# Optimization experiments

Measured on AMD Instinct MI355X. Metric: run time of the kernel, lower is better.

The kernel has to match this reference:

```python
import jax, jax.numpy as jnp
import numpy as np

NV, NQ, K, C, FF, H = 40000, 8192, 96, 128, 256, 8
DH = C // H


def _layernorm(x, g, b, eps=1e-5):
    m = jnp.mean(x, axis=-1, keepdims=True)
    v = jnp.var(x, axis=-1, keepdims=True)
    return (x - m) * jax.lax.rsqrt(v + eps) * g + b


def setup_inputs() -> dict:
    key = jax.random.key(0)
    ks = jax.random.split(key, 20)
    voxel_features = jax.random.normal(ks[0], (NV, C), dtype=jnp.float32)
    voxel_coords = jax.random.normal(ks[1], (NV, 3), dtype=jnp.float32)
    query_coords = jax.random.normal(ks[2], (NQ, 3), dtype=jnp.float32)
    raw = jax.random.randint(ks[3], (NQ, K), 0, 50000)
    key_indices = jnp.where(raw >= NV, -1, raw)  # -1 marks padded/missing keys
    key_indices = key_indices.at[:, 0].set(raw[:, 0] % NV)  # ensure >=1 valid key per query
    w = lambda k, shape: (jax.random.normal(k, shape, dtype=jnp.float32) * 0.02)
    return {
        "voxel_features": voxel_features,
        "voxel_coords": voxel_coords,
        "query_coords": query_coords,
        "key_indices": key_indices,
        "norm1_g": jnp.ones((C,), jnp.float32), "norm1_b": jnp.zeros((C,), jnp.float32),
        "q_pos_w": w(ks[4], (C, 3)), "q_pos_b": jnp.zeros((C,), jnp.float32),
        "k_pos_w": w(ks[5], (C, 3)), "k_pos_b": jnp.zeros((C,), jnp.float32),
        "in_w": w(ks[6], (3 * C, C)), "in_b": jnp.zeros((3 * C,), jnp.float32),
        "out_w": w(ks[7], (C, C)), "out_b": jnp.zeros((C,), jnp.float32),
        "norm2_g": jnp.ones((C,), jnp.float32), "norm2_b": jnp.zeros((C,), jnp.float32),
        "lin1_w": w(ks[8], (FF, C)), "lin1_b": jnp.zeros((FF,), jnp.float32),
        "lin2_w": w(ks[9], (C, FF)), "lin2_b": jnp.zeros((C,), jnp.float32),
        "fin_w": w(ks[10], (C, C)), "fin_b": jnp.zeros((C,), jnp.float32),
    }


def reference(voxel_features, voxel_coords, query_coords, key_indices,
              norm1_g, norm1_b, q_pos_w, q_pos_b, k_pos_w, k_pos_b,
              in_w, in_b, out_w, out_b, norm2_g, norm2_b,
              lin1_w, lin1_b, lin2_w, lin2_b, fin_w, fin_b):
    mask = key_indices < 0                      # [NQ, K] True = padded
    idx = jnp.where(mask, 0, key_indices)
    vf = _layernorm(voxel_features, norm1_g, norm1_b)   # norm1
    key_feat = vf[idx]                          # gather: [NQ, K, C]
    key_c = voxel_coords[idx]                   # [NQ, K, 3]
    # q_pos_proj: Linear(3,C)+ReLU ; k_pos_proj: Conv1d(3,C,1)+ReLU (== per-key linear)
    q_feat = jax.nn.relu(query_coords @ q_pos_w.T + q_pos_b)        # [NQ, C]
    key_pos = jax.nn.relu(jnp.einsum('nkt,ct->nkc', key_c, k_pos_w) + k_pos_b)
    key_feat = key_feat + key_pos               # [NQ, K, C]
    # nn.MultiheadAttention: query [1,NQ,C], key/value [K,NQ,C] -> per-query attention over K keys
    wq, wk, wv = in_w[:C], in_w[C:2 * C], in_w[2 * C:]
    bq, bk, bv = in_b[:C], in_b[C:2 * C], in_b[2 * C:]
    q = (q_feat @ wq.T + bq).reshape(NQ, H, DH)                 # [NQ,H,DH]
    k = (key_feat @ wk.T + bk).reshape(NQ, K, H, DH)            # [NQ,K,H,DH]
    v = (key_feat @ wv.T + bv).reshape(NQ, K, H, DH)
    scale = 1.0 / np.sqrt(DH)
    scores = jnp.einsum('nhd,nkhd->nhk', q, k) * scale          # [NQ,H,K]
    scores = jnp.where(mask[:, None, :], jnp.float32(-1e9), scores)
    attn = jax.nn.softmax(scores, axis=-1)
    ctx = jnp.einsum('nhk,nkhd->nhd', attn, v).reshape(NQ, C)
    attend = ctx @ out_w.T + out_b                              # [NQ,C]
    # FFN block (dropout=0 -> identity)
    h = _layernorm(attend, norm2_g, norm2_b)
    act = jax.nn.relu(h @ lin1_w.T + lin1_b) @ lin2_w.T + lin2_b
    x = attend + act
    out = jax.nn.relu(x @ fin_w.T + fin_b)                      # output_layer
    return out
```

## Files before the change

### kernel.cpp

```cpp
#include <hip/hip_runtime.h>
#include <hip/hip_bf16.h>
#include <math.h>

constexpr int NVOX = 40000;
constexpr int NQRY = 8192;
constexpr int KK   = 96;
constexpr int CH   = 128;
constexpr int FFD  = 256;

typedef __attribute__((ext_vector_type(8))) short short8;
typedef __attribute__((ext_vector_type(4))) float float4v;

__device__ inline float bflo(unsigned u) { return __uint_as_float(u << 16); }
__device__ inline float bfhi(unsigned u) { return __uint_as_float(u & 0xffff0000u); }
__device__ inline unsigned short f2bf(float x) {
  union { float f; unsigned u; } a; a.f = x;
  const unsigned r = a.u + 0x7fffu + ((a.u >> 16) & 1u);
  return (unsigned short)(r >> 16);
}
__device__ inline unsigned pack2(float lo, float hi) {
  return (unsigned)f2bf(lo) | ((unsigned)f2bf(hi) << 16);
}

__global__ __launch_bounds__(256) void k_prep(
    const float* __restrict__ vfeat, const float* __restrict__ vcoord,
    const float* __restrict__ n1g, const float* __restrict__ n1b,
    const float* __restrict__ kpw, const float* __restrict__ kpb,
    const float* __restrict__ in_w,
    const float* __restrict__ ow, const float* __restrict__ l1w,
    const float* __restrict__ l2w, const float* __restrict__ fw,
    __hip_bfloat16* __restrict__ Gb, __hip_bfloat16* __restrict__ Wb,
    __hip_bfloat16* __restrict__ Eb) {
  const int b = blockIdx.x;
  const int t = threadIdx.x;
  if (b < NVOX/16) {
    const int vloc = t >> 4;
    const int l    = t & 15;
    const int j = b * 16 + vloc;
    const float4* vrow = reinterpret_cast<const float4*>(vfeat + (size_t)j * CH);
    const float4 x0 = vrow[l*2], x1 = vrow[l*2+1];
    float s  = x0.x+x0.y+x0.z+x0.w + x1.x+x1.y+x1.z+x1.w;
    float ss = x0.x*x0.x+x0.y*x0.y+x0.z*x0.z+x0.w*x0.w
             + x1.x*x1.x+x1.y*x1.y+x1.z*x1.z+x1.w*x1.w;
    #pragma unroll
    for (int m = 8; m >= 1; m >>= 1) { s += __shfl_xor(s, m); ss += __shfl_xor(ss, m); }
    const float mean = s * (1.0f/CH);
    const float var  = ss * (1.0f/CH) - mean*mean;
    const float rstd = 1.0f / sqrtf(var + 1e-5f);
    const float c0 = vcoord[j*3+0], c1 = vcoord[j*3+1], c2 = vcoord[j*3+2];
    const float xv[8] = {x0.x,x0.y,x0.z,x0.w,x1.x,x1.y,x1.z,x1.w};
    float gv[8];
    #pragma unroll
    for (int u = 0; u < 8; u++) {
      const int c = l*8 + u;
      const float vf = (xv[u] - mean) * rstd * n1g[c] + n1b[c];
      const float kp = fmaf(c0, kpw[c*3+0], fmaf(c1, kpw[c*3+1], fmaf(c2, kpw[c*3+2], kpb[c])));
      gv[u] = vf + fmaxf(kp, 0.0f);
    }
    const uint4 pk = make_uint4(pack2(gv[0],gv[1]), pack2(gv[2],gv[3]),
                                pack2(gv[4],gv[5]), pack2(gv[6],gv[7]));
    *reinterpret_cast<uint4*>(Gb + (size_t)j*CH + l*8) = pk;
  } else {
    const int idx = b - NVOX/16;
    const float* src;
    __hip_bfloat16* dst;
    if (idx < 8) {
      const int e = (idx * 256 + t) * 16;
      src = in_w + (size_t)CH*CH + e;
      dst = Wb + e;
    } else {
      const int f = ((idx - 8) * 256 + t) * 16;
      dst = Eb + f;
      if      (f < 16384) src = ow  + f;
      else if (f < 49152) src = l1w + (f - 16384);
      else if (f < 81920) src = l2w + (f - 49152);
      else                src = fw  + (f - 81920);
    }
    float v[16];
    #pragma unroll
    for (int u = 0; u < 4; u++) {
      const float4 fq = *reinterpret_cast<const float4*>(src + u*4);
      v[u*4+0]=fq.x; v[u*4+1]=fq.y; v[u*4+2]=fq.z; v[u*4+3]=fq.w;
    }
    uint4* o = reinterpret_cast<uint4*>(dst);
    o[0] = make_uint4(pack2(v[0],v[1]), pack2(v[2],v[3]),
                      pack2(v[4],v[5]), pack2(v[6],v[7]));
    o[1] = make_uint4(pack2(v[8],v[9]), pack2(v[10],v[11]),
                      pack2(v[12],v[13]), pack2(v[14],v[15]));
  }
}

__global__ __launch_bounds__(256) void k_kv_gemm(
    const __hip_bfloat16* __restrict__ Gb, const __hip_bfloat16* __restrict__ Wb,
    const float* __restrict__ in_b,
    unsigned short* __restrict__ KVh) {
  __shared__ unsigned short ldsD[64][72];
  const int t = threadIdx.x;
  const int w = t >> 6;
  const int lane = t & 63;
  const int col = lane & 15;
  const int quad = lane >> 4;
  const int bx = blockIdx.x;
  const int v0 = (bx >> 2) * 64;
  const int cg = bx & 3;

  const unsigned short* gRow =
      reinterpret_cast<const unsigned short*>(Gb) + (size_t)(v0 + w*16 + col)*CH + quad*8;
  short8 afrag[4];
  #pragma unroll
  for (int kq = 0; kq < 4; kq++)
    afrag[kq] = *reinterpret_cast<const short8*>(gRow + kq*32);

  float4v acc[4];
  #pragma unroll
  for (int j = 0; j < 4; j++) {
    const float bia = in_b[CH + cg*64 + j*16 + col];
    acc[j] = (float4v){bia, bia, bia, bia};
  }
  const unsigned short* wB = reinterpret_cast<const unsigned short*>(Wb);
  #pragma unroll
  for (int kq = 0; kq < 4; kq++) {
    #pragma unroll
    for (int j = 0; j < 4; j++) {
      const short8 bfrag = *reinterpret_cast<const short8*>(
          wB + (size_t)(cg*64 + j*16 + col)*CH + kq*32 + quad*8);
      acc[j] = __builtin_amdgcn_mfma_f32_16x16x32_bf16(afrag[kq], bfrag, acc[j], 0, 0, 0);
    }
  }
  #pragma unroll
  for (int j = 0; j < 4; j++)
    #pragma unroll
    for (int r = 0; r < 4; r++)
      ldsD[w*16 + quad*4 + r][j*16 + col] = f2bf(acc[j][r]);
  __syncthreads();
  const int row = t >> 2;
  const int cc  = (t & 3) * 16;
  const uint4 d0 = *reinterpret_cast<const uint4*>(&ldsD[row][cc]);
  const uint4 d1 = *reinterpret_cast<const uint4*>(&ldsD[row][cc+8]);
  const int head = (cg & 1) * 4 + (cc >> 4);
  const int isV  = cg >> 1;
  unsigned short* dst = KVh + ((size_t)head*NVOX + (v0 + row))*32 + isV*16;
  uint4* out = reinterpret_cast<uint4*>(dst);
  out[0] = d0; out[1] = d1;
}

__global__ __launch_bounds__(256) void k_query(
    const float* __restrict__ qcoord,
    const float* __restrict__ qpw, const float* __restrict__ qpb,
    const float* __restrict__ in_w, const float* __restrict__ in_b,
    float* __restrict__ qout) {
  __shared__ float qf[16][CH];
  const int t = threadIdx.x;
  const int qbase = blockIdx.x * 16;
  #pragma unroll
  for (int i = 0; i < 8; i++) {
    const int e = t + 256*i;
    const int qv = e >> 7, c = e & 127;
    const int qq = qbase + qv;
    const float v = fmaf(qcoord[qq*3+0], qpw[c*3+0],
                    fmaf(qcoord[qq*3+1], qpw[c*3+1],
                    fmaf(qcoord[qq*3+2], qpw[c*3+2], qpb[c])));
    qf[qv][c] = fmaxf(v, 0.0f);
  }
  __syncthreads();
  const int oc = t & 127, half = t >> 7;
  const float* wrow = in_w + (size_t)oc * CH;
  const float bia = in_b[oc];
  float acc[8];
  #pragma unroll
  for (int v = 0; v < 8; v++) acc[v] = bia;
  for (int c = 0; c < CH; c += 4) {
    const float4 w4 = *reinterpret_cast<const float4*>(wrow + c);
    #pragma unroll
    for (int v = 0; v < 8; v++) {
      const float4 g4 = *reinterpret_cast<const float4*>(&qf[half*8+v][c]);
      acc[v] = fmaf(g4.x, w4.x, fmaf(g4.y, w4.y, fmaf(g4.z, w4.z, fmaf(g4.w, w4.w, acc[v]))));
    }
  }
  #pragma unroll
  for (int v = 0; v < 8; v++) qout[(size_t)(qbase + half*8 + v)*CH + oc] = acc[v];
}

__global__ __launch_bounds__(256) void k_attn(
    const unsigned short* __restrict__ KVh,
    const float* __restrict__ qg, const int* __restrict__ kidx,
    float* __restrict__ ctxg) {
  __shared__ float qs[8][16];
  __shared__ int   js[8*KK];
  __shared__ float sc[8*KK];
  __shared__ float red[4][8][16];
  __shared__ float rden[8];
  const int t  = threadIdx.x;
  const int h  = blockIdx.x & 7;
  const int n0 = (blockIdx.x >> 3) * 8;
  const unsigned short* KVbase = KVh + (size_t)h * NVOX * 32;

  #pragma unroll
  for (int i = 0; i < 3; i++)
    js[t + 256*i] = kidx[(size_t)n0*KK + t + 256*i];
  if (t < 128) {
    const int q = t >> 4, d = t & 15;
    qs[q][d] = qg[(size_t)(n0 + q)*CH + h*16 + d];
  }
  __syncthreads();
  #pragma unroll
  for (int i = 0; i < 3; i++) {
    const int e = t + 256*i;
    const int q = e / KK, k = e - q*KK;
    const int j = js[e];
    float s;
    if (j < 0) {
      s = -1e9f;
    } else {
      const uint4* kr = reinterpret_cast<const uint4*>(KVbase + (size_t)j*32);
      const uint4 ka = kr[0], kb = kr[1];
      const float* qh = qs[q];
      s = 0.0f;
      s = fmaf(qh[0],  bflo(ka.x), s); s = fmaf(qh[1],  bfhi(ka.x), s);
      s = fmaf(qh[2],  bflo(ka.y), s); s = fmaf(qh[3],  bfhi(ka.y), s);
      s = fmaf(qh[4],  bflo(ka.z), s); s = fmaf(qh[5],  bfhi(ka.z), s);
      s = fmaf(qh[6],  bflo(ka.w), s); s = fmaf(qh[7],  bfhi(ka.w), s);
      s = fmaf(qh[8],  bflo(kb.x), s); s = fmaf(qh[9],  bfhi(kb.x), s);
      s = fmaf(qh[10], bflo(kb.y), s); s = fmaf(qh[11], bfhi(kb.y), s);
      s = fmaf(qh[12], bflo(kb.z), s); s = fmaf(qh[13], bfhi(kb.z), s);
      s = fmaf(qh[14], bflo(kb.w), s); s = fmaf(qh[15], bfhi(kb.w), s);
      s *= 0.25f;
    }
    sc[e] = s;
  }
  __syncthreads();
  if (t < 128) {
    const int q = t >> 4, l = t & 15;
    float mx = -3e38f;
    for (int k = l; k < KK; k += 16) mx = fmaxf(mx, sc[q*KK + k]);
    #pragma unroll
    for (int m = 8; m >= 1; m >>= 1) mx = fmaxf(mx, __shfl_xor(mx, m));
    float sum = 0.0f;
    for (int k = l; k < KK; k += 16) {
      const float p = __expf(sc[q*KK + k] - mx);
      sc[q*KK + k] = p;
      sum += p;
    }
    #pragma unroll
    for (int m = 8; m >= 1; m >>= 1) sum += __shfl_xor(sum, m);
    if (l == 0) rden[q] = 1.0f / sum;
  }
  __syncthreads();
  {
    const int q = t >> 5, cp = (t >> 2) & 7, kg = t & 3;
    float a0 = 0.0f, a1 = 0.0f;
    const int k0 = kg * 24;
    for (int k = k0; k < k0 + 24; k++) {
      const int j = js[q*KK + k];
      if (j >= 0) {
        const unsigned vv = *reinterpret_cast<const unsigned*>(
            KVbase + (size_t)j*32 + 16 + cp*2);
        const float w = sc[q*KK + k];
        a0 = fmaf(w, bflo(vv), a0);
        a1 = fmaf(w, bfhi(vv), a1);
      }
    }
    *reinterpret_cast<float2*>(&red[kg][q][cp*2]) = make_float2(a0, a1);
  }
  __syncthreads();
  if (t < 128) {
    const int q = t >> 4, d = t & 15;
    ctxg[(size_t)(n0 + q)*CH + h*16 + d] =
        (red[0][q][d] + red[1][q][d] + red[2][q][d] + red[3][q][d]) * rden[q];
  }
}

__global__ __launch_bounds__(256) void k_epi(
    const float* __restrict__ ctxg, const __hip_bfloat16* __restrict__ Eb,
    const float* __restrict__ ob,
    const float* __restrict__ n2g, const float* __restrict__ n2b,
    const float* __restrict__ l1b, const float* __restrict__ l2b,
    const float* __restrict__ fb,
    float* __restrict__ outp) {
  __shared__ unsigned short csb[16][136];
  __shared__ float attnS[16][132];
  __shared__ unsigned short hb[16][136];
  __shared__ unsigned short a1b[16][264];
  __shared__ unsigned short xb[16][136];
  const unsigned short* owb  = reinterpret_cast<const unsigned short*>(Eb);
  const unsigned short* l1wb = owb + 16384;
  const unsigned short* l2wb = owb + 49152;
  const unsigned short* fwb  = owb + 81920;

  const int t = threadIdx.x;
  const int w = t >> 6;
  const int lane = t & 63;
  const int col = lane & 15;
  const int quad = lane >> 4;
  const int qbase = blockIdx.x * 16;

  {
    const int e = t * 8;
    const int row = e >> 7, cc = e & 127;
    const float4* src = reinterpret_cast<const float4*>(ctxg + (size_t)(qbase+row)*CH + cc);
    const float4 x0 = src[0], x1 = src[1];
    *reinterpret_cast<uint4*>(&csb[row][cc]) =
        make_uint4(pack2(x0.x,x0.y), pack2(x0.z,x0.w), pack2(x1.x,x1.y), pack2(x1.z,x1.w));
  }
  __syncthreads();
  {
    short8 af[4];
    #pragma unroll
    for (int kq = 0; kq < 4; kq++)
      af[kq] = *reinterpret_cast<const short8*>(&csb[col][quad*8 + kq*32]);
    #pragma unroll
    for (int j = 0; j < 2; j++) {
      const int n0 = w*32 + j*16;
      const float bia = ob[n0 + col];
      float4v acc = (float4v){bia, bia, bia, bia};
      #pragma unroll
      for (int kq = 0; kq < 4; kq++) {
        const short8 bf = *reinterpret_cast<const short8*>(
            owb + (size_t)(n0 + col)*CH + kq*32 + quad*8);
        acc = __builtin_amdgcn_mfma_f32_16x16x32_bf16(af[kq], bf, acc, 0, 0, 0);
      }
      #pragma unroll
      for (int r = 0; r < 4; r++) attnS[quad*4 + r][n0 + col] = acc[r];
    }
  }
  __syncthreads();
  {
    const int row = t >> 4, l = t & 15;
    float s = 0.0f, ss = 0.0f;
    #pragma unroll
    for (int c = l; c < CH; c += 16) { const float x = attnS[row][c]; s += x; ss += x*x; }
    #pragma unroll
    for (int m = 8; m >= 1; m >>= 1) { s += __shfl_xor(s, m); ss += __shfl_xor(ss, m); }
    const float mean = s * (1.0f/CH);
    const float var  = ss * (1.0f/CH) - mean*mean;
    const float rstd = 1.0f / sqrtf(var + 1e-5f);
    #pragma unroll
    for (int c = l; c < CH; c += 16)
      hb[row][c] = f2bf((attnS[row][c] - mean) * rstd * n2g[c] + n2b[c]);
  }
  __syncthreads();
  {
    short8 af[4];
    #pragma unroll
    for (int kq = 0; kq < 4; kq++)
      af[kq] = *reinterpret_cast<const short8*>(&hb[col][quad*8 + kq*32]);
    #pragma unroll
    for (int j = 0; j < 4; j++) {
      const int n0 = w*64 + j*16;
      const float bia = l1b[n0 + col];
      float4v acc = (float4v){bia, bia, bia, bia};
      #pragma unroll
      for (int kq = 0; kq < 4; kq++) {
        const short8 bf = *reinterpret_cast<const short8*>(
            l1wb + (size_t)(n0 + col)*CH + kq*32 + quad*8);
        acc = __builtin_amdgcn_mfma_f32_16x16x32_bf16(af[kq], bf, acc, 0, 0, 0);
      }
      #pragma unroll
      for (int r = 0; r < 4; r++)
        a1b[quad*4 + r][n0 + col] = f2bf(fmaxf(acc[r], 0.0f));
    }
  }
  __syncthreads();
  {
    short8 af[8];
    #pragma unroll
    for (int kq = 0; kq < 8; kq++)
      af[kq] = *reinterpret_cast<const short8*>(&a1b[col][quad*8 + kq*32]);
    #pragma unroll
    for (int j = 0; j < 2; j++) {
      const int n0 = w*32 + j*16;
      const float bia = l2b[n0 + col];
      float4v acc = (float4v){bia, bia, bia, bia};
      #pragma unroll
      for (int kq = 0; kq < 8; kq++) {
        const short8 bf = *reinterpret_cast<const short8*>(
            l2wb + (size_t)(n0 + col)*FFD + kq*32 + quad*8);
        acc = __builtin_amdgcn_mfma_f32_16x16x32_bf16(af[kq], bf, acc, 0, 0, 0);
      }
      #pragma unroll
      for (int r = 0; r < 4; r++)
        xb[quad*4 + r][n0 + col] = f2bf(acc[r] + attnS[quad*4 + r][n0 + col]);
    }
  }
  __syncthreads();
  {
    short8 af[4];
    #pragma unroll
    for (int kq = 0; kq < 4; kq++)
      af[kq] = *reinterpret_cast<const short8*>(&xb[col][quad*8 + kq*32]);
    #pragma unroll
    for (int j = 0; j < 2; j++) {
      const int n0 = w*32 + j*16;
      const float bia = fb[n0 + col];
      float4v acc = (float4v){bia, bia, bia, bia};
      #pragma unroll
      for (int kq = 0; kq < 4; kq++) {
        const short8 bf = *reinterpret_cast<const short8*>(
            fwb + (size_t)(n0 + col)*CH + kq*32 + quad*8);
        acc = __builtin_amdgcn_mfma_f32_16x16x32_bf16(af[kq], bf, acc, 0, 0, 0);
      }
      #pragma unroll
      for (int r = 0; r < 4; r++)
        outp[(size_t)(qbase + quad*4 + r)*CH + n0 + col] = fmaxf(acc[r], 0.0f);
    }
  }
}

extern "C" void kernel_launch(void* const* d_in, const int* in_sizes, int n_in,
                              void* d_out, int out_size, void* d_ws, size_t ws_size,
                              hipStream_t stream) {
  const float* vfeat  = (const float*)d_in[0];
  const float* vcoord = (const float*)d_in[1];
  const float* qcoord = (const float*)d_in[2];
  const int*   kidx   = (const int*)  d_in[3];
  const float* n1g    = (const float*)d_in[4];
  const float* n1b    = (const float*)d_in[5];
  const float* qpw    = (const float*)d_in[6];
  const float* qpb    = (const float*)d_in[7];
  const float* kpw    = (const float*)d_in[8];
  const float* kpb    = (const float*)d_in[9];
  const float* in_w   = (const float*)d_in[10];
  const float* in_b   = (const float*)d_in[11];
  const float* out_w  = (const float*)d_in[12];
  const float* out_b  = (const float*)d_in[13];
  const float* n2g    = (const float*)d_in[14];
  const float* n2b    = (const float*)d_in[15];
  const float* l1w    = (const float*)d_in[16];
  const float* l1b    = (const float*)d_in[17];
  const float* l2w    = (const float*)d_in[18];
  const float* l2b    = (const float*)d_in[19];
  const float* fw     = (const float*)d_in[20];
  const float* fb     = (const float*)d_in[21];
  float* out = (float*)d_out;

  unsigned short* KVh = (unsigned short*)d_ws;
  __hip_bfloat16* Gb = (__hip_bfloat16*)(KVh + (size_t)8*NVOX*32);
  __hip_bfloat16* Wb = Gb + (size_t)NVOX*CH;
  __hip_bfloat16* Eb = Wb + (size_t)2*CH*CH;
  float* qb = (float*)(Eb + 98304);
  float* cx = qb + (size_t)NQRY*CH;

  k_prep   <<<NVOX/16 + 32, 256, 0, stream>>>(vfeat, vcoord, n1g, n1b, kpw, kpb,
                                              in_w, out_w, l1w, l2w, fw, Gb, Wb, Eb);
  k_query  <<<NQRY/16, 256, 0, stream>>>(qcoord, qpw, qpb, in_w, in_b, qb);
  k_kv_gemm<<<(NVOX/64)*4, 256, 0, stream>>>(Gb, Wb, in_b, KVh);
  k_attn   <<<(NQRY/8)*8, 256, 0, stream>>>(KVh, qb, kidx, cx);
  k_epi    <<<NQRY/16, 256, 0, stream>>>(cx, Eb, out_b, n2g, n2b, l1b, l2b, fb, out);
}
```

Measured before the change: 226.6 us.

## Load each key/value row once into registers and reuse it for scores and context

The attention kernel now has each group of 4 lanes load a full 64-byte K/V row with coalesced 16-byte loads. All 12 rows per thread are issued up front and kept in registers. Scores are computed from those registers with a lane shuffle, and the same registers are reused for the weighted V sum. This removes the second gather of V from global memory and the staging of key indices in shared memory. The cost is higher register pressure (48 extra VGPRs for the buffer) and more redundant FMAs on masked keys, which are clamped to row 0.

Result: faster. 209.6 us (-7.5%).

```diff
diff --git a/kernel.cpp b/kernel.cpp
--- a/kernel.cpp
+++ b/kernel.cpp
@@ -186,59 +186,63 @@
     const float* __restrict__ qg, const int* __restrict__ kidx,
     float* __restrict__ ctxg) {
   __shared__ float qs[8][16];
-  __shared__ int   js[8*KK];
-  __shared__ float sc[8*KK];
-  __shared__ float red[4][8][16];
+  __shared__ float sc[8*104];
+  __shared__ float red[128][9];
   __shared__ float rden[8];
-  const int t  = threadIdx.x;
-  const int h  = blockIdx.x & 7;
-  const int n0 = (blockIdx.x >> 3) * 8;
+  const int t    = threadIdx.x;
+  const int h    = blockIdx.x & 7;
+  const int n0   = (blockIdx.x >> 3) * 8;
+  const int w    = t >> 6;
+  const int lane = t & 63;
+  const int quad = lane >> 2;
+  const int r    = lane & 3;
+  const int qh   = quad >> 3;
+  const int g    = quad & 7;
+  const int q_l  = 2*w + qh;
   const unsigned short* KVbase = KVh + (size_t)h * NVOX * 32;
 
-  #pragma unroll
-  for (int i = 0; i < 3; i++)
-    js[t + 256*i] = kidx[(size_t)n0*KK + t + 256*i];
   if (t < 128) {
     const int q = t >> 4, d = t & 15;
     qs[q][d] = qg[(size_t)(n0 + q)*CH + h*16 + d];
   }
-  __syncthreads();
-  #pragma unroll
-  for (int i = 0; i < 3; i++) {
-    const int e = t + 256*i;
-    const int q = e / KK, k = e - q*KK;
-    const int j = js[e];
-    float s;
-    if (j < 0) {
-      s = -1e9f;
-    } else {
-      const uint4* kr = reinterpret_cast<const uint4*>(KVbase + (size_t)j*32);
-      const uint4 ka = kr[0], kb = kr[1];
-      const float* qh = qs[q];
-      s = 0.0f;
-      s = fmaf(qh[0],  bflo(ka.x), s); s = fmaf(qh[1],  bfhi(ka.x), s);
-      s = fmaf(qh[2],  bflo(ka.y), s); s = fmaf(qh[3],  bfhi(ka.y), s);
-      s = fmaf(qh[4],  bflo(ka.z), s); s = fmaf(qh[5],  bfhi(ka.z), s);
-      s = fmaf(qh[6],  bflo(ka.w), s); s = fmaf(qh[7],  bfhi(ka.w), s);
-      s = fmaf(qh[8],  bflo(kb.x), s); s = fmaf(qh[9],  bfhi(kb.x), s);
-      s = fmaf(qh[10], bflo(kb.y), s); s = fmaf(qh[11], bfhi(kb.y), s);
-      s = fmaf(qh[12], bflo(kb.z), s); s = fmaf(qh[13], bfhi(kb.z), s);
-      s = fmaf(qh[14], bflo(kb.w), s); s = fmaf(qh[15], bfhi(kb.w), s);
-      s *= 0.25f;
-    }
-    sc[e] = s;
+  unsigned msk = 0;
+  uint4 kvbuf[12];
+  const int krow = (n0 + q_l)*KK + g;
+  #pragma unroll
+  for (int it = 0; it < 12; it++) {
+    const int j0 = kidx[krow + it*8];
+    msk |= (unsigned)(j0 < 0) << it;
+    const int j = (j0 < 0) ? 0 : j0;
+    kvbuf[it] = *reinterpret_cast<const uint4*>(KVbase + (size_t)j*32 + r*8);
+  }
+  __syncthreads();
+  const float4 qa = *reinterpret_cast<const float4*>(&qs[q_l][(r & 1)*8]);
+  const float4 qb = *reinterpret_cast<const float4*>(&qs[q_l][(r & 1)*8 + 4]);
+  #pragma unroll
+  for (int it = 0; it < 12; it++) {
+    const uint4 kv = kvbuf[it];
+    float s = 0.0f;
+    s = fmaf(qa.x, bflo(kv.x), s); s = fmaf(qa.y, bfhi(kv.x), s);
+    s = fmaf(qa.z, bflo(kv.y), s); s = fmaf(qa.w, bfhi(kv.y), s);
+    s = fmaf(qb.x, bflo(kv.z), s); s = fmaf(qb.y, bfhi(kv.z), s);
+    s = fmaf(qb.z, bflo(kv.w), s); s = fmaf(qb.w, bfhi(kv.w), s);
+    s += __shfl_xor(s, 1);
+    if (r == 0)
+      sc[q_l*104 + g + it*8] = ((msk >> it) & 1) ? -1e9f : s * 0.25f;
   }
   __syncthreads();
   if (t < 128) {
     const int q = t >> 4, l = t & 15;
     float mx = -3e38f;
-    for (int k = l; k < KK; k += 16) mx = fmaxf(mx, sc[q*KK + k]);
+    #pragma unroll
+    for (int k = l; k < KK; k += 16) mx = fmaxf(mx, sc[q*104 + k]);
     #pragma unroll
     for (int m = 8; m >= 1; m >>= 1) mx = fmaxf(mx, __shfl_xor(mx, m));
     float sum = 0.0f;
+    #pragma unroll
     for (int k = l; k < KK; k += 16) {
-      const float p = __expf(sc[q*KK + k] - mx);
-      sc[q*KK + k] = p;
+      const float p = __expf(sc[q*104 + k] - mx);
+      sc[q*104 + k] = p;
       sum += p;
     }
     #pragma unroll
@@ -247,26 +251,30 @@
   }
   __syncthreads();
   {
-    const int q = t >> 5, cp = (t >> 2) & 7, kg = t & 3;
-    float a0 = 0.0f, a1 = 0.0f;
-    const int k0 = kg * 24;
-    for (int k = k0; k < k0 + 24; k++) {
-      const int j = js[q*KK + k];
-      if (j >= 0) {
-        const unsigned vv = *reinterpret_cast<const unsigned*>(
-            KVbase + (size_t)j*32 + 16 + cp*2);
-        const float w = sc[q*KK + k];
-        a0 = fmaf(w, bflo(vv), a0);
-        a1 = fmaf(w, bfhi(vv), a1);
-      }
-    }
-    *reinterpret_cast<float2*>(&red[kg][q][cp*2]) = make_float2(a0, a1);
+    float acc[8] = {0,0,0,0,0,0,0,0};
+    #pragma unroll
+    for (int it = 0; it < 12; it++) {
+      const float wg = sc[q_l*104 + g + it*8];
+      const uint4 kv = kvbuf[it];
+      acc[0] = fmaf(wg, bflo(kv.x), acc[0]); acc[1] = fmaf(wg, bfhi(kv.x), acc[1]);
+      acc[2] = fmaf(wg, bflo(kv.y), acc[2]); acc[3] = fmaf(wg, bfhi(kv.y), acc[3]);
+      acc[4] = fmaf(wg, bflo(kv.z), acc[4]); acc[5] = fmaf(wg, bfhi(kv.z), acc[5]);
+      acc[6] = fmaf(wg, bflo(kv.w), acc[6]); acc[7] = fmaf(wg, bfhi(kv.w), acc[7]);
+    }
+    if (r >= 2) {
+      const int slot = q_l*16 + g*2 + (r - 2);
+      #pragma unroll
+      for (int u = 0; u < 8; u++) red[slot][u] = acc[u];
+    }
   }
   __syncthreads();
   if (t < 128) {
     const int q = t >> 4, d = t & 15;
-    ctxg[(size_t)(n0 + q)*CH + h*16 + d] =
-        (red[0][q][d] + red[1][q][d] + red[2][q][d] + red[3][q][d]) * rden[q];
+    const int half = d >> 3, u = d & 7;
+    float s = 0.0f;
+    #pragma unroll
+    for (int gg = 0; gg < 8; gg++) s += red[q*16 + gg*2 + half][u];
+    ctxg[(size_t)(n0 + q)*CH + h*16 + d] = s * rden[q];
   }
 }
 
```
